# Kernel optimization log

Measured on AMD Instinct MI355X. Metric: run time of the kernel, lower is better.

## Reference

```python
import jax, jax.numpy as jnp
import numpy as np

T_B = 0.9   # GIoU threshold
T_C = 0.2   # KL threshold
EPS = 1e-9
LOGIT_EPS = 1e-6

def box_cxcywh_to_xyxy(b):
    cx, cy, w, h = b[..., 0], b[..., 1], b[..., 2], b[..., 3]
    return jnp.stack([cx - 0.5 * w, cy - 0.5 * h, cx + 0.5 * w, cy + 0.5 * h], axis=-1)

def pairwise_giou(boxes):
    # boxes: [n, 4] xyxy -> [n, n] generalized IoU
    area = (boxes[:, 2] - boxes[:, 0]) * (boxes[:, 3] - boxes[:, 1])  # [n]
    lt = jnp.maximum(boxes[:, None, :2], boxes[None, :, :2])   # [n, n, 2]
    rb = jnp.minimum(boxes[:, None, 2:], boxes[None, :, 2:])
    wh = jnp.clip(rb - lt, 0.0)
    inter = wh[..., 0] * wh[..., 1]                              # [n, n]
    union = area[:, None] + area[None, :] - inter
    iou = inter / (union + EPS)
    # smallest enclosing box
    lt_e = jnp.minimum(boxes[:, None, :2], boxes[None, :, :2])
    rb_e = jnp.maximum(boxes[:, None, 2:], boxes[None, :, 2:])
    wh_e = jnp.clip(rb_e - lt_e, 0.0)
    area_e = wh_e[..., 0] * wh_e[..., 1]
    return iou - (area_e - union) / (area_e + EPS)

def build_aggregation_mask(bboxes_i, logits_i):
    # bboxes_i: [n_q, 4] cxcywh; logits_i: [n_q, C]. All non-differentiable.
    n_q = bboxes_i.shape[0]
    giou = pairwise_giou(box_cxcywh_to_xyxy(bboxes_i))           # [n_q, n_q]
    iou_gt = giou > T_B
    # pairwise KL between per-query (normalized) class distributions
    p = jax.nn.sigmoid(logits_i)
    q = p / (jnp.sum(p, axis=-1, keepdims=True) + EPS)           # [n_q, C]
    logq = jnp.log(q + EPS)
    self_ent = jnp.sum(q * logq, axis=-1)                        # [n_q]
    kl = self_ent[:, None] - q @ logq.T                          # kl[i,j] = KL(q_i || q_j)
    kl_lt = kl < T_C
    mask = iou_gt & kl_lt
    mask = mask | mask.T                                         # symmetrize
    # transitive closure via repeated boolean squaring (log2(n_q)+1 iters suffice)
    adj = mask.astype(jnp.float32)
    n_iters = int(np.ceil(np.log2(n_q))) + 1
    for _ in range(n_iters):
        adj = ((adj + adj @ adj) > 0).astype(jnp.float32)
    # dedup clusters: keep row i only if i is the smallest member of its cluster
    adj_bool = adj > 0
    first_member = jnp.argmax(adj_bool, axis=1)                  # first True per row
    keep = (first_member == jnp.arange(n_q)).astype(jnp.float32)
    return adj * keep[:, None]                                   # [n_q, n_q] float32

def aggregate_one(bboxes_i, logits_i):
    agg_mask = jax.lax.stop_gradient(
        build_aggregation_mask(jax.lax.stop_gradient(bboxes_i),
                               jax.lax.stop_gradient(logits_i)))
    denom = jnp.maximum(jnp.sum(agg_mask, axis=-1, keepdims=True), 1.0)  # [n_q, 1]
    agg_bboxes = (agg_mask @ bboxes_i) / denom                   # [n_q, 4]
    prob = jax.nn.sigmoid(logits_i)
    agg_prob = (agg_mask @ prob) / denom                         # [n_q, C]
    agg_prob = jnp.clip(agg_prob, LOGIT_EPS, 1.0 - LOGIT_EPS)
    agg_logits = jnp.log(agg_prob) - jnp.log1p(-agg_prob)        # logit with eps
    return agg_bboxes, agg_logits

def setup_inputs() -> dict:
    key = jax.random.key(0)
    k1, k2 = jax.random.split(key)
    bboxes = jax.random.uniform(k1, (64, 900, 4), dtype=jnp.float32)
    logits = jax.random.normal(k2, (64, 900, 91), dtype=jnp.float32)
    return {"bboxes": bboxes, "logits": logits}

def reference(bboxes, logits):
    return jax.vmap(aggregate_one)(bboxes, logits)
```

## Files before the change

### kernel.cpp

```cpp
#include <hip/hip_runtime.h>
#include <math.h>

#define NB 64
#define NQ 900
#define NC 91
#define TB_THR 0.9f
#define TC_THR 0.2f
#define EPSF 1e-9f
#define LGEPS 1e-6f

#define TPB 256
#define TT 120
#define SUB 60
#define TPAIRS 36
#define EDGE_BLOCKS (NB * TPAIRS)
#define INIT_BLOCKS 225
#define SP_BLOCKS 225
#define OUT4_BLOCKS 5344
#define SLOT 64

__device__ __forceinline__ int uf_find(int* p, int x) {
    volatile int* vp = (volatile int*)p;
    int px = vp[x];
    while (px != x) { x = px; px = vp[x]; }
    return x;
}

__device__ void uf_unite(int* p, int a, int b) {
    while (true) {
        a = uf_find(p, a);
        b = uf_find(p, b);
        if (a == b) return;
        int hi = a > b ? a : b;
        int lo = a ^ b ^ hi;
        if (atomicCAS(&p[hi], hi, lo) == hi) return;
        a = hi; b = lo;
    }
}

__device__ __forceinline__ bool pair_test(float4 R, float ai, float4 B, float aj) {
    float ltx = fmaxf(R.x, B.x), lty = fmaxf(R.y, B.y);
    float rbx = fminf(R.z, B.z), rby = fminf(R.w, B.w);
    float w = fmaxf(rbx - ltx, 0.f), h = fmaxf(rby - lty, 0.f);
    float inter = w * h;
    float uni = ai + aj - inter;
    if (!(inter > TB_THR * (uni + EPSF))) return false;
    float ex = fmaxf(fmaxf(R.z, B.z) - fminf(R.x, B.x), 0.f);
    float ey = fmaxf(fmaxf(R.w, B.w) - fminf(R.y, B.y), 0.f);
    float ae = ex * ey;
    float iou = inter / (uni + EPSF);
    float giou = iou - (ae - uni) / (ae + EPSF);
    return giou > TB_THR;
}

__device__ void kl_process(unsigned long long m, int ibase, int j, int gbase,
                           const float* __restrict__ logits, int lane,
                           int* lcnt, int2* lbuf) {
    while (m) {
        int src = __ffsll((long long)m) - 1; m &= m - 1;
        int gi = gbase + ibase + src;
        int gj = gbase + j;
        const float* li = logits + (size_t)gi * NC;
        const float* lj = logits + (size_t)gj * NC;
        int c1 = lane + 64;
        bool h1 = (c1 < NC);
        float pi0 = 1.f / (1.f + expf(-li[lane]));
        float pj0 = 1.f / (1.f + expf(-lj[lane]));
        float pi1 = h1 ? 1.f / (1.f + expf(-li[c1])) : 0.f;
        float pj1 = h1 ? 1.f / (1.f + expf(-lj[c1])) : 0.f;
        float si = pi0 + pi1, sj = pj0 + pj1;
        for (int o = 32; o; o >>= 1) { si += __shfl_xor(si, o); sj += __shfl_xor(sj, o); }
        float di = si + EPSF, dj = sj + EPSF;
        float qi0 = pi0 / di, qi1 = pi1 / di, qj0 = pj0 / dj, qj1 = pj1 / dj;
        float lqi0 = logf(qi0 + EPSF), lqj0 = logf(qj0 + EPSF);
        float lqi1 = h1 ? logf(qi1 + EPSF) : 0.f;
        float lqj1 = h1 ? logf(qj1 + EPSF) : 0.f;
        float ei  = qi0 * lqi0 + (h1 ? qi1 * lqi1 : 0.f);
        float ej  = qj0 * lqj0 + (h1 ? qj1 * lqj1 : 0.f);
        float dij = qi0 * lqj0 + (h1 ? qi1 * lqj1 : 0.f);
        float dji = qj0 * lqi0 + (h1 ? qj1 * lqi1 : 0.f);
        for (int o = 32; o; o >>= 1) {
            ei  += __shfl_xor(ei, o);  ej  += __shfl_xor(ej, o);
            dij += __shfl_xor(dij, o); dji += __shfl_xor(dji, o);
        }
        bool edge = ((ei - dij) < TC_THR) || ((ej - dji) < TC_THR);
        if (edge && lane == 0) {
            int pos = atomicAdd(lcnt, 1);
            if (pos < SLOT) lbuf[pos] = make_int2(gi, gj);
        }
    }
}

__global__ __launch_bounds__(TPB)
void k_sweep(const float* __restrict__ bboxes, const float* __restrict__ logits,
             int* __restrict__ parent, int* __restrict__ ovl,
             int* __restrict__ bcnt, int2* __restrict__ slots) {
    __shared__ float4 jb[TT];
    __shared__ float  ja[TT];
    __shared__ int lcnt;
    __shared__ int2 lbuf[SLOT];
    int bid = blockIdx.x;
    if (bid >= EDGE_BLOCKS) {
        int idx = (bid - EDGE_BLOCKS) * TPB + threadIdx.x;
        if (idx < NB * NQ) { parent[idx] = idx; ovl[idx] = 0; }
        return;
    }
    if (threadIdx.x == 0) lcnt = 0;
    int b = bid / TPAIRS, tp = bid % TPAIRS;
    int tj = (int)((sqrtf(8.f * tp + 1.f) - 1.f) * 0.5f);
    while ((tj + 1) * (tj + 2) / 2 <= tp) ++tj;
    while (tj * (tj + 1) / 2 > tp) --tj;
    int ti = tp - tj * (tj + 1) / 2;
    int i0 = ti * TT, j0 = tj * TT;
    const float4* bb = (const float4*)(bboxes + (size_t)b * NQ * 4);

    int jend = NQ - j0; if (jend > TT) jend = TT;
    for (int k = threadIdx.x; k < jend; k += TPB) {
        float4 v = bb[j0 + k];
        float4 e = make_float4(v.x - 0.5f * v.z, v.y - 0.5f * v.w,
                               v.x + 0.5f * v.z, v.y + 0.5f * v.w);
        jb[k] = e;
        ja[k] = (e.z - e.x) * (e.w - e.y);
    }
    __syncthreads();

    int lane = threadIdx.x & 63;
    int wv   = threadIdx.x >> 6;
    bool lv  = lane < SUB;
    int iA = i0 + (lv ? lane : 0);
    int iB = iA + SUB;
    bool vB = lv && (iB < NQ);

    float4 a4 = bb[iA];
    float4 RA = make_float4(a4.x - 0.5f * a4.z, a4.y - 0.5f * a4.w,
                            a4.x + 0.5f * a4.z, a4.y + 0.5f * a4.w);
    float aA = (RA.z - RA.x) * (RA.w - RA.y);
    float4 b4 = bb[vB ? iB : iA];
    float4 RB = make_float4(b4.x - 0.5f * b4.z, b4.y - 0.5f * b4.w,
                            b4.x + 0.5f * b4.z, b4.y + 0.5f * b4.w);
    float aB = (RB.z - RB.x) * (RB.w - RB.y);

    int gbase = b * NQ;
    int jlo = wv * 30, jhi = jlo + 30; if (jhi > jend) jhi = jend;
    for (int jj = jlo; jj < jhi; ++jj) {
        int j = j0 + jj;
        float4 B = jb[jj];
        float aj = ja[jj];
        bool fA = lv && (iA < j) && pair_test(RA, aA, B, aj);
        bool fB = vB && (iB < j) && pair_test(RB, aB, B, aj);
        unsigned long long mA = __ballot(fA);
        unsigned long long mB = __ballot(fB);
        if (mA | mB) {
            kl_process(mA, i0, j, gbase, logits, lane, &lcnt, lbuf);
            kl_process(mB, i0 + SUB, j, gbase, logits, lane, &lcnt, lbuf);
        }
    }
    __syncthreads();
    int n = lcnt < SLOT ? lcnt : SLOT;
    if (threadIdx.x == 0) bcnt[bid] = n;
    for (int k = threadIdx.x; k < n; k += TPB) slots[bid * SLOT + k] = lbuf[k];
}

__global__ __launch_bounds__(TPB)
void k_unite(int* __restrict__ parent, int* __restrict__ ovl,
             const int* __restrict__ bcnt, const int2* __restrict__ slots) {
    int blk = blockIdx.x * TPB + threadIdx.x;
    if (blk >= EDGE_BLOCKS) return;
    int c = bcnt[blk]; if (c > SLOT) c = SLOT;
    for (int k = 0; k < c; ++k) {
        int2 e = slots[blk * SLOT + k];
        uf_unite(parent, e.x, e.y);
        ovl[e.x] = 1;
        ovl[e.y] = 1;
    }
}

__global__ __launch_bounds__(TPB)
void k_out(const float* __restrict__ bboxes, const float* __restrict__ logits,
           int* __restrict__ parent, const int* __restrict__ ovl,
           float* __restrict__ out) {
    const long long NBB  = (long long)NB * NQ * 4;
    const long long NTOT = NBB + (long long)NB * NQ * NC;
    const float LO = logf(LGEPS) - log1pf(-LGEPS);
    const float HI = logf(1.f - LGEPS) - log1pf(-(1.f - LGEPS));
    int bid = blockIdx.x;
    if (bid < SP_BLOCKS) {
        int wv   = bid * 4 + (threadIdx.x >> 6);
        int lane = threadIdx.x & 63;
        int r0   = wv * 64;
        int r    = r0 + lane;
        bool inEdge = ovl[r] != 0;
        bool isroot = inEdge && (uf_find(parent, r) == r);
        unsigned long long mask = __ballot(isroot);
        while (mask) {
            int bit = __ffsll((long long)mask) - 1; mask &= mask - 1;
            int R = r0 + bit;
            int b = R / NQ;
            int base = b * NQ;
            float a0 = 0.f, a1 = 0.f, ab = 0.f;
            int cm = 0;
            for (int it = 0; it < 15; ++it) {
                int row = it * 64 + lane;
                int g = base + row;
                bool mem = (row < NQ) && (ovl[g] != 0) && (uf_find(parent, g) == R);
                unsigned long long mm = __ballot(mem);
                cm += __popcll(mm);
                while (mm) {
                    int mb = __ffsll((long long)mm) - 1; mm &= mm - 1;
                    int gg = base + it * 64 + mb;
                    const float* lg = logits + (size_t)gg * NC;
                    a0 += 1.f / (1.f + expf(-lg[lane]));
                    if (lane + 64 < NC) a1 += 1.f / (1.f + expf(-lg[lane + 64]));
                    if (lane < 4)       ab += bboxes[(size_t)gg * 4 + lane];
                }
            }
            float d = (float)cm;
            if (lane < 4) out[(size_t)R * 4 + lane] = ab / d;
            float v0 = fminf(fmaxf(a0 / d, LGEPS), 1.f - LGEPS);
            out[NBB + (size_t)R * NC + lane] = logf(v0) - log1pf(-v0);
            if (lane + 64 < NC) {
                float v1 = fminf(fmaxf(a1 / d, LGEPS), 1.f - LGEPS);
                out[NBB + (size_t)R * NC + lane + 64] = logf(v1) - log1pf(-v1);
            }
        }
        return;
    }
    long long q4 = (long long)(bid - SP_BLOCKS) * TPB + threadIdx.x;
    if (q4 >= NTOT / 4) return;
    long long idx = q4 * 4;
    if (idx < NBB) {
        int g = (int)(idx >> 2);
        float4 o;
        if (ovl[g] == 0) o = ((const float4*)bboxes)[g];
        else if (uf_find(parent, g) != g) o = make_float4(0.f, 0.f, 0.f, 0.f);
        else return;
        ((float4*)out)[q4] = o;
        return;
    }
    long long t = idx - NBB;
    int g0 = (int)(t / NC), g3 = (int)((t + 3) / NC);
    if (g0 == g3) {
        float4 o;
        if (ovl[g0] == 0) {
            float4 L = *(const float4*)(logits + t);
            o = make_float4(fminf(fmaxf(L.x, LO), HI), fminf(fmaxf(L.y, LO), HI),
                            fminf(fmaxf(L.z, LO), HI), fminf(fmaxf(L.w, LO), HI));
        } else if (uf_find(parent, g0) != g0) o = make_float4(LO, LO, LO, LO);
        else return;
        ((float4*)out)[q4] = o;
    } else {
#pragma unroll
        for (int e = 0; e < 4; ++e) {
            long long te = t + e;
            int g = (int)(te / NC);
            if (ovl[g] == 0) out[idx + e] = fminf(fmaxf(logits[te], LO), HI);
            else if (uf_find(parent, g) != g) out[idx + e] = LO;
        }
    }
}

extern "C" void kernel_launch(void* const* d_in, const int* in_sizes, int n_in,
                              void* d_out, int out_size, void* d_ws, size_t ws_size,
                              hipStream_t stream) {
    const float* bboxes = (const float*)d_in[0];
    const float* logits = (const float*)d_in[1];
    float* out = (float*)d_out;

    char* ws = (char*)d_ws;
    const int NROWS = NB * NQ;
    int*  parent = (int*) (ws);
    int*  ovl    = (int*) (ws + 1 * NROWS * 4);
    int*  bcnt   = (int*) (ws + 2 * NROWS * 4);
    int2* slots  = (int2*)(ws + 2 * NROWS * 4 + 16384);

    k_sweep<<<EDGE_BLOCKS + INIT_BLOCKS, TPB, 0, stream>>>(
        bboxes, logits, parent, ovl, bcnt, slots);

    k_unite<<<(EDGE_BLOCKS + TPB - 1) / TPB, TPB, 0, stream>>>(parent, ovl, bcnt, slots);

    k_out<<<SP_BLOCKS + OUT4_BLOCKS, TPB, 0, stream>>>(bboxes, logits, parent, ovl, out);
}
```

Measured before the change: 55.37 us.

## Replace tiled all-pairs sweep with per-batch spatial grid and in-block union-find

Each batch is now handled by one 1024-thread block. Boxes are bucketed into a 10x10 grid of centre cells, and each box tests only the boxes in neighbouring cells. This relies on the GIoU>0.9 threshold implying close centres. Candidate pairs then run the KL test, and union-find happens in shared memory before a packed root/flag label is written. This removes the separate unite kernel and the global parent/ovl arrays, and cuts the O(n^2) pair tests. The cost is that only 64 blocks run, which risks low GPU occupancy. The 256-slot candidate buffer can also overflow silently.

```diff
diff --git a/kernel.cpp b/kernel.cpp
--- a/kernel.cpp
+++ b/kernel.cpp
@@ -10,26 +10,22 @@
 #define LGEPS 1e-6f
 
 #define TPB 256
-#define TT 120
-#define SUB 60
-#define TPAIRS 36
-#define EDGE_BLOCKS (NB * TPAIRS)
-#define INIT_BLOCKS 225
+#define TPB_S 1024
+#define SLOTB 256
 #define SP_BLOCKS 225
 #define OUT4_BLOCKS 5344
-#define SLOT 64
-
-__device__ __forceinline__ int uf_find(int* p, int x) {
+
+__device__ __forceinline__ int ufl_find(int* p, int x) {
     volatile int* vp = (volatile int*)p;
     int px = vp[x];
     while (px != x) { x = px; px = vp[x]; }
     return x;
 }
 
-__device__ void uf_unite(int* p, int a, int b) {
+__device__ void ufl_unite(int* p, int a, int b) {
     while (true) {
-        a = uf_find(p, a);
-        b = uf_find(p, b);
+        a = ufl_find(p, a);
+        b = ufl_find(p, b);
         if (a == b) return;
         int hi = a > b ? a : b;
         int lo = a ^ b ^ hi;
@@ -53,15 +49,96 @@
     return giou > TB_THR;
 }
 
-__device__ void kl_process(unsigned long long m, int ibase, int j, int gbase,
-                           const float* __restrict__ logits, int lane,
-                           int* lcnt, int2* lbuf) {
-    while (m) {
-        int src = __ffsll((long long)m) - 1; m &= m - 1;
-        int gi = gbase + ibase + src;
-        int gj = gbase + j;
-        const float* li = logits + (size_t)gi * NC;
-        const float* lj = logits + (size_t)gj * NC;
+__global__ __launch_bounds__(TPB_S)
+void k_sweep(const float* __restrict__ bboxes, const float* __restrict__ logits,
+             int* __restrict__ label) {
+    __shared__ float4 xy[NQ];
+    __shared__ float  ar[NQ];
+    __shared__ short  cellOf[NQ];
+    __shared__ int    perm[NQ];
+    __shared__ int    cstart[101];
+    __shared__ int    coff[128];
+    __shared__ int    cnt[100];
+    __shared__ int    up[NQ];
+    __shared__ unsigned char ef[NQ];
+    __shared__ int    lcnt;
+    __shared__ int2   lbuf[SLOTB];
+
+    int b   = blockIdx.x;
+    int tid = threadIdx.x;
+    const float4* bb = (const float4*)(bboxes + (size_t)b * NQ * 4);
+
+    if (tid < 100) cnt[tid] = 0;
+    if (tid == 0) lcnt = 0;
+    __syncthreads();
+
+    if (tid < NQ) {
+        int i = tid;
+        float4 v = bb[i];
+        float4 e = make_float4(v.x - 0.5f * v.z, v.y - 0.5f * v.w,
+                               v.x + 0.5f * v.z, v.y + 0.5f * v.w);
+        xy[i] = e;
+        ar[i] = (e.z - e.x) * (e.w - e.y);
+        int bx = (int)(v.x * 10.f); bx = bx < 0 ? 0 : (bx > 9 ? 9 : bx);
+        int by = (int)(v.y * 10.f); by = by < 0 ? 0 : (by > 9 ? 9 : by);
+        int c = by * 10 + bx;
+        cellOf[i] = (short)c;
+        atomicAdd(&cnt[c], 1);
+        up[i] = i;
+        ef[i] = 0;
+    }
+    __syncthreads();
+
+    if (tid < 100) coff[tid] = cnt[tid];
+    __syncthreads();
+    for (int off = 1; off < 128; off <<= 1) {
+        int v = 0;
+        if (tid < 100 && tid >= off) v = coff[tid - off];
+        __syncthreads();
+        if (tid < 100) coff[tid] += v;
+        __syncthreads();
+    }
+    if (tid < 100) cstart[tid + 1] = coff[tid];
+    if (tid == 0) cstart[0] = 0;
+    __syncthreads();
+    if (tid < 100) coff[tid] = cstart[tid];
+    __syncthreads();
+    if (tid < NQ) {
+        int c = cellOf[tid];
+        int pos = atomicAdd(&coff[c], 1);
+        perm[pos] = tid;
+    }
+    __syncthreads();
+
+    if (tid < NQ) {
+        int i = tid;
+        float4 R = xy[i]; float ai_ = ar[i];
+        int c = cellOf[i], bx = c % 10, by = c / 10;
+        int xlo = bx > 0 ? bx - 1 : 0, xhi = bx < 9 ? bx + 1 : 9;
+        int ylo = by > 0 ? by - 1 : 0, yhi = by < 9 ? by + 1 : 9;
+        for (int yy = ylo; yy <= yhi; ++yy)
+        for (int xx = xlo; xx <= xhi; ++xx) {
+            int d = yy * 10 + xx;
+            int s1 = cstart[d + 1];
+            for (int k = cstart[d]; k < s1; ++k) {
+                int j = perm[k];
+                if (j <= i) continue;
+                if (pair_test(R, ai_, xy[j], ar[j])) {
+                    int pos = atomicAdd(&lcnt, 1);
+                    if (pos < SLOTB) lbuf[pos] = make_int2(i, j);
+                }
+            }
+        }
+    }
+    __syncthreads();
+
+    int n = lcnt < SLOTB ? lcnt : SLOTB;
+    int wv = tid >> 6, lane = tid & 63;
+    int gbase = b * NQ;
+    for (int m = wv; m < n; m += 16) {
+        int2 pr = lbuf[m];
+        const float* li = logits + (size_t)(gbase + pr.x) * NC;
+        const float* lj = logits + (size_t)(gbase + pr.y) * NC;
         int c1 = lane + 64;
         bool h1 = (c1 < NC);
         float pi0 = 1.f / (1.f + expf(-li[lane]));
@@ -85,100 +162,23 @@
         }
         bool edge = ((ei - dij) < TC_THR) || ((ej - dji) < TC_THR);
         if (edge && lane == 0) {
-            int pos = atomicAdd(lcnt, 1);
-            if (pos < SLOT) lbuf[pos] = make_int2(gi, gj);
-        }
-    }
-}
-
-__global__ __launch_bounds__(TPB)
-void k_sweep(const float* __restrict__ bboxes, const float* __restrict__ logits,
-             int* __restrict__ parent, int* __restrict__ ovl,
-             int* __restrict__ bcnt, int2* __restrict__ slots) {
-    __shared__ float4 jb[TT];
-    __shared__ float  ja[TT];
-    __shared__ int lcnt;
-    __shared__ int2 lbuf[SLOT];
-    int bid = blockIdx.x;
-    if (bid >= EDGE_BLOCKS) {
-        int idx = (bid - EDGE_BLOCKS) * TPB + threadIdx.x;
-        if (idx < NB * NQ) { parent[idx] = idx; ovl[idx] = 0; }
-        return;
-    }
-    if (threadIdx.x == 0) lcnt = 0;
-    int b = bid / TPAIRS, tp = bid % TPAIRS;
-    int tj = (int)((sqrtf(8.f * tp + 1.f) - 1.f) * 0.5f);
-    while ((tj + 1) * (tj + 2) / 2 <= tp) ++tj;
-    while (tj * (tj + 1) / 2 > tp) --tj;
-    int ti = tp - tj * (tj + 1) / 2;
-    int i0 = ti * TT, j0 = tj * TT;
-    const float4* bb = (const float4*)(bboxes + (size_t)b * NQ * 4);
-
-    int jend = NQ - j0; if (jend > TT) jend = TT;
-    for (int k = threadIdx.x; k < jend; k += TPB) {
-        float4 v = bb[j0 + k];
-        float4 e = make_float4(v.x - 0.5f * v.z, v.y - 0.5f * v.w,
-                               v.x + 0.5f * v.z, v.y + 0.5f * v.w);
-        jb[k] = e;
-        ja[k] = (e.z - e.x) * (e.w - e.y);
-    }
-    __syncthreads();
-
-    int lane = threadIdx.x & 63;
-    int wv   = threadIdx.x >> 6;
-    bool lv  = lane < SUB;
-    int iA = i0 + (lv ? lane : 0);
-    int iB = iA + SUB;
-    bool vB = lv && (iB < NQ);
-
-    float4 a4 = bb[iA];
-    float4 RA = make_float4(a4.x - 0.5f * a4.z, a4.y - 0.5f * a4.w,
-                            a4.x + 0.5f * a4.z, a4.y + 0.5f * a4.w);
-    float aA = (RA.z - RA.x) * (RA.w - RA.y);
-    float4 b4 = bb[vB ? iB : iA];
-    float4 RB = make_float4(b4.x - 0.5f * b4.z, b4.y - 0.5f * b4.w,
-                            b4.x + 0.5f * b4.z, b4.y + 0.5f * b4.w);
-    float aB = (RB.z - RB.x) * (RB.w - RB.y);
-
-    int gbase = b * NQ;
-    int jlo = wv * 30, jhi = jlo + 30; if (jhi > jend) jhi = jend;
-    for (int jj = jlo; jj < jhi; ++jj) {
-        int j = j0 + jj;
-        float4 B = jb[jj];
-        float aj = ja[jj];
-        bool fA = lv && (iA < j) && pair_test(RA, aA, B, aj);
-        bool fB = vB && (iB < j) && pair_test(RB, aB, B, aj);
-        unsigned long long mA = __ballot(fA);
-        unsigned long long mB = __ballot(fB);
-        if (mA | mB) {
-            kl_process(mA, i0, j, gbase, logits, lane, &lcnt, lbuf);
-            kl_process(mB, i0 + SUB, j, gbase, logits, lane, &lcnt, lbuf);
-        }
-    }
-    __syncthreads();
-    int n = lcnt < SLOT ? lcnt : SLOT;
-    if (threadIdx.x == 0) bcnt[bid] = n;
-    for (int k = threadIdx.x; k < n; k += TPB) slots[bid * SLOT + k] = lbuf[k];
-}
-
-__global__ __launch_bounds__(TPB)
-void k_unite(int* __restrict__ parent, int* __restrict__ ovl,
-             const int* __restrict__ bcnt, const int2* __restrict__ slots) {
-    int blk = blockIdx.x * TPB + threadIdx.x;
-    if (blk >= EDGE_BLOCKS) return;
-    int c = bcnt[blk]; if (c > SLOT) c = SLOT;
-    for (int k = 0; k < c; ++k) {
-        int2 e = slots[blk * SLOT + k];
-        uf_unite(parent, e.x, e.y);
-        ovl[e.x] = 1;
-        ovl[e.y] = 1;
+            ef[pr.x] = 1;
+            ef[pr.y] = 1;
+            ufl_unite(up, pr.x, pr.y);
+        }
+    }
+    __syncthreads();
+
+    if (tid < NQ) {
+        int r = tid;
+        while (up[r] != r) r = up[r];
+        label[gbase + tid] = ((gbase + r) << 1) | (ef[tid] ? 1 : 0);
     }
 }
 
 __global__ __launch_bounds__(TPB)
 void k_out(const float* __restrict__ bboxes, const float* __restrict__ logits,
-           int* __restrict__ parent, const int* __restrict__ ovl,
-           float* __restrict__ out) {
+           const int* __restrict__ label, float* __restrict__ out) {
     const long long NBB  = (long long)NB * NQ * 4;
     const long long NTOT = NBB + (long long)NB * NQ * NC;
     const float LO = logf(LGEPS) - log1pf(-LGEPS);
@@ -189,8 +189,8 @@
         int lane = threadIdx.x & 63;
         int r0   = wv * 64;
         int r    = r0 + lane;
-        bool inEdge = ovl[r] != 0;
-        bool isroot = inEdge && (uf_find(parent, r) == r);
+        int lv   = label[r];
+        bool isroot = (lv & 1) && ((lv >> 1) == r);
         unsigned long long mask = __ballot(isroot);
         while (mask) {
             int bit = __ffsll((long long)mask) - 1; mask &= mask - 1;
@@ -201,8 +201,7 @@
             int cm = 0;
             for (int it = 0; it < 15; ++it) {
                 int row = it * 64 + lane;
-                int g = base + row;
-                bool mem = (row < NQ) && (ovl[g] != 0) && (uf_find(parent, g) == R);
+                bool mem = (row < NQ) && ((label[base + row] >> 1) == R);
                 unsigned long long mm = __ballot(mem);
                 cm += __popcll(mm);
                 while (mm) {
@@ -230,9 +229,10 @@
     long long idx = q4 * 4;
     if (idx < NBB) {
         int g = (int)(idx >> 2);
+        int v = label[g];
         float4 o;
-        if (ovl[g] == 0) o = ((const float4*)bboxes)[g];
-        else if (uf_find(parent, g) != g) o = make_float4(0.f, 0.f, 0.f, 0.f);
+        if (!(v & 1))            o = ((const float4*)bboxes)[g];
+        else if ((v >> 1) != g)  o = make_float4(0.f, 0.f, 0.f, 0.f);
         else return;
         ((float4*)out)[q4] = o;
         return;
@@ -240,12 +240,13 @@
     long long t = idx - NBB;
     int g0 = (int)(t / NC), g3 = (int)((t + 3) / NC);
     if (g0 == g3) {
+        int v = label[g0];
         float4 o;
-        if (ovl[g0] == 0) {
+        if (!(v & 1)) {
             float4 L = *(const float4*)(logits + t);
             o = make_float4(fminf(fmaxf(L.x, LO), HI), fminf(fmaxf(L.y, LO), HI),
                             fminf(fmaxf(L.z, LO), HI), fminf(fmaxf(L.w, LO), HI));
-        } else if (uf_find(parent, g0) != g0) o = make_float4(LO, LO, LO, LO);
+        } else if ((v >> 1) != g0) o = make_float4(LO, LO, LO, LO);
         else return;
         ((float4*)out)[q4] = o;
     } else {
@@ -253,8 +254,9 @@
         for (int e = 0; e < 4; ++e) {
             long long te = t + e;
             int g = (int)(te / NC);
-            if (ovl[g] == 0) out[idx + e] = fminf(fmaxf(logits[te], LO), HI);
-            else if (uf_find(parent, g) != g) out[idx + e] = LO;
+            int v = label[g];
+            if (!(v & 1))           out[idx + e] = fminf(fmaxf(logits[te], LO), HI);
+            else if ((v >> 1) != g) out[idx + e] = LO;
         }
     }
 }
@@ -265,18 +267,9 @@
     const float* bboxes = (const float*)d_in[0];
     const float* logits = (const float*)d_in[1];
     float* out = (float*)d_out;
-
-    char* ws = (char*)d_ws;
-    const int NROWS = NB * NQ;
-    int*  parent = (int*) (ws);
-    int*  ovl    = (int*) (ws + 1 * NROWS * 4);
-    int*  bcnt   = (int*) (ws + 2 * NROWS * 4);
-    int2* slots  = (int2*)(ws + 2 * NROWS * 4 + 16384);
-
-    k_sweep<<<EDGE_BLOCKS + INIT_BLOCKS, TPB, 0, stream>>>(
-        bboxes, logits, parent, ovl, bcnt, slots);
-
-    k_unite<<<(EDGE_BLOCKS + TPB - 1) / TPB, TPB, 0, stream>>>(parent, ovl, bcnt, slots);
-
-    k_out<<<SP_BLOCKS + OUT4_BLOCKS, TPB, 0, stream>>>(bboxes, logits, parent, ovl, out);
-}
+    int* label = (int*)d_ws;
+
+    k_sweep<<<NB, TPB_S, 0, stream>>>(bboxes, logits, label);
+
+    k_out<<<SP_BLOCKS + OUT4_BLOCKS, TPB, 0, stream>>>(bboxes, logits, label, out);
+}
```

New measurement: 59.08 us. +6.7%, slower.
